# Kernel tuning notes

Measured on AMD Instinct MI355X. Metric: run time of the kernel, lower is better.

The kernel has to match this reference:

```python
import jax, jax.numpy as jnp
import numpy as np

NOPE = 128          # qk_nope_head_dim
ROPE = 64           # qk_rope_head_dim
KV_LORA = 512       # kv_lora_rank
SCALE = (KV_LORA + ROPE) ** (-0.5)


def setup_inputs() -> dict:
    key = jax.random.key(0)
    k1, k2, k3, k4, k5 = jax.random.split(key, 5)
    T, H, K, S = 512, 128, 512, 8192
    q = jax.random.normal(k1, (T, H, NOPE + ROPE), dtype=jnp.float32)
    kv_cache = jax.random.normal(k2, (S, KV_LORA + ROPE), dtype=jnp.float32)
    topk_indices = jax.random.randint(k3, (T, K), 0, S, dtype=jnp.int32)
    k_b_proj_trans = jax.random.normal(k4, (H, KV_LORA, NOPE), dtype=jnp.float32) * 0.02
    v_b_proj = jax.random.normal(k5, (H, 128, KV_LORA), dtype=jnp.float32) * 0.02
    return {"q": q, "kv_cache": kv_cache, "topk_indices": topk_indices,
            "k_b_proj_trans": k_b_proj_trans, "v_b_proj": v_b_proj}


def reference(q, kv_cache, topk_indices, k_b_proj_trans, v_b_proj):
    # q: [T, H, 192]; kv_cache: [S, 576]; topk_indices: [T, K]
    q_nope, q_rope = q[..., :NOPE], q[..., NOPE:]
    # bmm_out(q_nope_t, k_b_proj_trans.transpose(1,2)): [T,H,128] x [H,512,128] -> [T,H,512]
    q_lat = jnp.einsum('thd,hkd->thk', q_nope, k_b_proj_trans)
    q_concat = jnp.concatenate([q_lat, q_rope], axis=-1)        # [T, H, 576]
    # sparse MLA: gather selected latent KV per token
    kv_sel = kv_cache[topk_indices]                              # [T, K, 576]
    scores = jnp.einsum('thc,tkc->thk', q_concat, kv_sel) * SCALE
    p = jax.nn.softmax(scores, axis=-1)                          # [T, H, K]
    attn_lat = jnp.einsum('thk,tkc->thc', p, kv_sel[..., :KV_LORA])  # [T, H, 512]
    # bmm_out(attn_lat_t, v_b_proj.transpose(1,2)): [T,H,512] x [H,512,128] -> [T,H,128]
    out = jnp.einsum('thc,hvc->thv', attn_lat, v_b_proj)
    return out
```

## Files before the change

kernel.cpp:

```cpp
#include <hip/hip_runtime.h>
#include <stdint.h>


#define SCALE 0.041666666666666664f

typedef __bf16 bf16x8 __attribute__((ext_vector_type(8)));
typedef float floatx4 __attribute__((ext_vector_type(4)));

static __device__ __forceinline__ unsigned short f2bf(float f) {
  unsigned int u = __builtin_bit_cast(unsigned int, f);
  u += 0x7FFF + ((u >> 16) & 1);
  return (unsigned short)(u >> 16);
}
static __device__ __forceinline__ float bf2f(unsigned short h) {
  unsigned int u = ((unsigned int)h) << 16;
  return __builtin_bit_cast(float, u);
}
static __device__ __forceinline__ unsigned int pack2(float lo, float hi) {
  return (unsigned int)f2bf(lo) | ((unsigned int)f2bf(hi) << 16);
}
static __device__ __forceinline__ void ldsdma16(const void* g, void* l) {
  __builtin_amdgcn_global_load_lds(
      (const __attribute__((address_space(1))) void*)g,
      (__attribute__((address_space(3))) void*)l, 16, 0, 0);
}
static __device__ __forceinline__ void stage8_f32(const float* __restrict__ src,
                                                  unsigned short* dst) {
  const float4* s4 = reinterpret_cast<const float4*>(src);
  float4 v0 = s4[0], v1 = s4[1];
  uint4 o;
  o.x = pack2(v0.x, v0.y); o.y = pack2(v0.z, v0.w);
  o.z = pack2(v1.x, v1.y); o.w = pack2(v1.z, v1.w);
  *reinterpret_cast<uint4*>(dst) = o;
}

static __device__ __forceinline__ void mfma_4x4(const unsigned short* As,
                                                const unsigned short* Bs,
                                                int wm, int wn, int l15, int quad,
                                                floatx4 acc[4][4]) {
  bf16x8 af[4], bfr[4];
#pragma unroll
  for (int i = 0; i < 4; ++i)
    af[i] = *reinterpret_cast<const bf16x8*>(&As[(wm + i * 16 + l15) * 32 + quad * 8]);
#pragma unroll
  for (int j = 0; j < 4; ++j)
    bfr[j] = *reinterpret_cast<const bf16x8*>(&Bs[(wn + j * 16 + l15) * 32 + quad * 8]);
#pragma unroll
  for (int i = 0; i < 4; ++i)
#pragma unroll
    for (int j = 0; j < 4; ++j)
      acc[i][j] = __builtin_amdgcn_mfma_f32_16x16x32_bf16(af[i], bfr[j], acc[i][j], 0, 0, 0);
}

__global__ void prep(const float* __restrict__ kv, unsigned short* __restrict__ kvb,
                     const float* __restrict__ q, unsigned short* __restrict__ qc) {
  int b = blockIdx.x;
  if (b < 4608) {
    int i = b * 256 + threadIdx.x;
    float4 v = reinterpret_cast<const float4*>(kv)[i];
    ushort4 o;
    o.x = f2bf(v.x); o.y = f2bf(v.y); o.z = f2bf(v.z); o.w = f2bf(v.w);
    reinterpret_cast<ushort4*>(kvb)[i] = o;
  } else {
    int i = (b - 4608) * 256 + threadIdx.x;
    int r = i & 63;
    int th = i >> 6;
    qc[(size_t)th * 576 + 512 + r] = f2bf(q[(size_t)th * 192 + 128 + r] * SCALE);
  }
}

__global__ __launch_bounds__(256) void qlat_gemm(const float* __restrict__ q,
                                                 const float* __restrict__ kb,
                                                 unsigned short* __restrict__ qc) {
  const int h = blockIdx.x;
  const int tm = (blockIdx.y & 3) * 128;
  const int tn = (blockIdx.y >> 2) * 128;
  __shared__ __align__(16) unsigned short As[128 * 32];
  __shared__ __align__(16) unsigned short Bs[128 * 32];
  const int tid = threadIdx.x;
  const int lane = tid & 63, wave = tid >> 6;
  const int wm = (wave & 1) * 64, wn = (wave >> 1) * 64;
  const int l15 = lane & 15, quad = lane >> 4;
  const int r0 = tid >> 2, cg = tid & 3;
  const float* a0 = q + ((size_t)(tm + r0) * 128 + h) * 192 + cg * 8;
  const float* a1 = q + ((size_t)(tm + r0 + 64) * 128 + h) * 192 + cg * 8;
  const float* b0 = kb + ((size_t)h * 512 + tn + r0) * 128 + cg * 8;
  const float* b1 = b0 + (size_t)64 * 128;
  floatx4 acc[4][4] = {};
  for (int ks = 0; ks < 4; ++ks) {
    stage8_f32(a0 + ks * 32, &As[tid * 8]);
    stage8_f32(a1 + ks * 32, &As[2048 + tid * 8]);
    stage8_f32(b0 + ks * 32, &Bs[tid * 8]);
    stage8_f32(b1 + ks * 32, &Bs[2048 + tid * 8]);
    __syncthreads();
    mfma_4x4(As, Bs, wm, wn, l15, quad, acc);
    __syncthreads();
  }
#pragma unroll
  for (int i = 0; i < 4; ++i) {
    const int row = wm + i * 16 + quad * 4;
#pragma unroll
    for (int j = 0; j < 4; ++j) {
      const int col = wn + j * 16 + l15;
#pragma unroll
      for (int r = 0; r < 4; ++r) {
        const int t = tm + row + r;
        qc[((size_t)t * 128 + h) * 576 + tn + col] = f2bf(acc[i][j][r] * SCALE);
      }
    }
  }
}

__global__ __launch_bounds__(256) void scores_gemm(const unsigned short* __restrict__ qc,
                                                   const unsigned short* __restrict__ kvb,
                                                   const int* __restrict__ topk,
                                                   unsigned short* __restrict__ P) {
  const int t = blockIdx.x;
  const int tn = blockIdx.y * 128;
  __shared__ __align__(16) unsigned short As[128 * 32];
  __shared__ __align__(16) unsigned short Bs[128 * 32];
  const int tid = threadIdx.x;
  const int lane = tid & 63, wave = tid >> 6;
  const int wm = (wave & 1) * 64, wn = (wave >> 1) * 64;
  const int l15 = lane & 15, quad = lane >> 4;
  const int r0 = tid >> 2, cg = tid & 3;
  const unsigned short* a0 = qc + ((size_t)t * 128 + r0) * 576 + cg * 8;
  const unsigned short* a1 = a0 + (size_t)64 * 576;
  const int idx0 = topk[t * 512 + tn + r0];
  const int idx1 = topk[t * 512 + tn + r0 + 64];
  const unsigned short* b0 = kvb + (size_t)idx0 * 576 + cg * 8;
  const unsigned short* b1 = kvb + (size_t)idx1 * 576 + cg * 8;
  floatx4 acc[4][4] = {};
  for (int ks = 0; ks < 18; ++ks) {
    ldsdma16(a0 + ks * 32, &As[tid * 8]);
    ldsdma16(a1 + ks * 32, &As[2048 + tid * 8]);
    ldsdma16(b0 + ks * 32, &Bs[tid * 8]);
    ldsdma16(b1 + ks * 32, &Bs[2048 + tid * 8]);
    __syncthreads();
    mfma_4x4(As, Bs, wm, wn, l15, quad, acc);
    __syncthreads();
  }
#pragma unroll
  for (int i = 0; i < 4; ++i) {
    const int row = wm + i * 16 + quad * 4;
#pragma unroll
    for (int j = 0; j < 4; ++j) {
      const int col = tn + wn + j * 16 + l15;
#pragma unroll
      for (int r = 0; r < 4; ++r)
        P[((size_t)t * 128 + row + r) * 512 + col] = f2bf(acc[i][j][r]);
    }
  }
}

__global__ __launch_bounds__(256) void softmax_rows(const unsigned short* __restrict__ Pin,
                                                    unsigned short* __restrict__ P2) {
  const int row = blockIdx.x * 4 + (threadIdx.x >> 6);
  const int t = row >> 7, h = row & 127;
  const int lane = threadIdx.x & 63;
  const unsigned short* rp = Pin + (size_t)row * 512 + lane * 8;
  uint4 raw = *reinterpret_cast<const uint4*>(rp);
  unsigned int w[4] = {raw.x, raw.y, raw.z, raw.w};
  float f[8];
  float mx = -1e30f;
#pragma unroll
  for (int i = 0; i < 8; ++i) {
    f[i] = bf2f((unsigned short)((w[i >> 1] >> ((i & 1) * 16)) & 0xFFFF));
    mx = fmaxf(mx, f[i]);
  }
#pragma unroll
  for (int off = 32; off; off >>= 1) mx = fmaxf(mx, __shfl_xor(mx, off, 64));
  float s = 0.f;
#pragma unroll
  for (int i = 0; i < 8; ++i) { f[i] = __expf(f[i] - mx); s += f[i]; }
#pragma unroll
  for (int off = 32; off; off >>= 1) s += __shfl_xor(s, off, 64);
  const float inv = 1.0f / s;
  uint4 o;
  o.x = pack2(f[0] * inv, f[1] * inv);
  o.y = pack2(f[2] * inv, f[3] * inv);
  o.z = pack2(f[4] * inv, f[5] * inv);
  o.w = pack2(f[6] * inv, f[7] * inv);
  unsigned short* wp =
      P2 + (((size_t)t * 16 + (lane >> 2)) * 128 + h) * 32 + (lane & 3) * 8;
  *reinterpret_cast<uint4*>(wp) = o;
}

#define BSTRIDE 40
__global__ __launch_bounds__(256) void attn_gemm(const unsigned short* __restrict__ P2,
                                                 const unsigned short* __restrict__ kvb,
                                                 const int* __restrict__ topk,
                                                 unsigned short* __restrict__ alat) {
  const int t = blockIdx.x;
  const int tn = blockIdx.y * 128;
  __shared__ __align__(16) unsigned short St[2][32 * 128];
  __shared__ __align__(16) unsigned short Bs[128 * BSTRIDE];
  const int tid = threadIdx.x;
  const int lane = tid & 63, wave = tid >> 6;
  const int wm = (wave & 1) * 64, wn = (wave >> 1) * 64;
  const int l15 = lane & 15, quad = lane >> 4;
  const int key0 = tid >> 4;
  const int cs = tid & 15;
  const int kgT = tid & 3;
  const int cp = tid >> 2;
  const int* tkrow = topk + t * 512;
  const unsigned short* a_base =
      P2 + ((size_t)t * 16 * 128 + wm + l15) * 32 + quad * 8;
  floatx4 acc[4][4] = {};
  bf16x8 a_cur[4], a_nxt[4];
  {
    const int i0 = tkrow[key0];
    const int i1 = tkrow[16 + key0];
    ldsdma16(kvb + (size_t)i0 * 576 + tn + cs * 8, &St[0][tid * 8]);
    ldsdma16(kvb + (size_t)i1 * 576 + tn + cs * 8, &St[0][2048 + tid * 8]);
#pragma unroll
    for (int i = 0; i < 4; ++i)
      a_cur[i] = *reinterpret_cast<const bf16x8*>(a_base + (size_t)i * 16 * 32);
  }
  __syncthreads();
  int cur = 0;
  for (int ks = 0; ks < 16; ++ks) {
    unsigned int w[8];
#pragma unroll
    for (int i = 0; i < 8; ++i)
      w[i] = *reinterpret_cast<const unsigned int*>(
          &St[cur][(kgT * 8 + i) * 128 + cp * 2]);
    unsigned short r0[8], r1[8];
#pragma unroll
    for (int i = 0; i < 8; ++i) {
      r0[i] = (unsigned short)(w[i] & 0xFFFF);
      r1[i] = (unsigned short)(w[i] >> 16);
    }
    *reinterpret_cast<uint4*>(&Bs[(2 * cp) * BSTRIDE + kgT * 8]) =
        *reinterpret_cast<const uint4*>(r0);
    *reinterpret_cast<uint4*>(&Bs[(2 * cp + 1) * BSTRIDE + kgT * 8]) =
        *reinterpret_cast<const uint4*>(r1);
    __syncthreads();
    if (ks < 15) {
      const int i0 = tkrow[(ks + 1) * 32 + key0];
      const int i1 = tkrow[(ks + 1) * 32 + 16 + key0];
      ldsdma16(kvb + (size_t)i0 * 576 + tn + cs * 8, &St[cur ^ 1][tid * 8]);
      ldsdma16(kvb + (size_t)i1 * 576 + tn + cs * 8, &St[cur ^ 1][2048 + tid * 8]);
#pragma unroll
      for (int i = 0; i < 4; ++i)
        a_nxt[i] = *reinterpret_cast<const bf16x8*>(
            a_base + ((size_t)(ks + 1) * 128 + i * 16) * 32);
    }
    bf16x8 bfr[4];
#pragma unroll
    for (int j = 0; j < 4; ++j)
      bfr[j] = *reinterpret_cast<const bf16x8*>(
          &Bs[(wn + j * 16 + l15) * BSTRIDE + quad * 8]);
#pragma unroll
    for (int i = 0; i < 4; ++i)
#pragma unroll
      for (int j = 0; j < 4; ++j)
        acc[i][j] =
            __builtin_amdgcn_mfma_f32_16x16x32_bf16(a_cur[i], bfr[j], acc[i][j], 0, 0, 0);
    __syncthreads();
#pragma unroll
    for (int i = 0; i < 4; ++i) a_cur[i] = a_nxt[i];
    cur ^= 1;
  }
#pragma unroll
  for (int i = 0; i < 4; ++i) {
    const int row = wm + i * 16 + quad * 4;
#pragma unroll
    for (int j = 0; j < 4; ++j) {
      const int col = tn + wn + j * 16 + l15;
#pragma unroll
      for (int r = 0; r < 4; ++r)
        alat[((size_t)(row + r) * 512 + t) * 512 + col] = f2bf(acc[i][j][r]);
    }
  }
}

__global__ __launch_bounds__(256) void out_gemm(const unsigned short* __restrict__ alat,
                                                const float* __restrict__ vb,
                                                float* __restrict__ out) {
  const int h = blockIdx.x;
  const int tm = blockIdx.y * 128;
  __shared__ __align__(16) unsigned short As[128 * 32];
  __shared__ __align__(16) unsigned short Bs[128 * 32];
  const int tid = threadIdx.x;
  const int lane = tid & 63, wave = tid >> 6;
  const int wm = (wave & 1) * 64, wn = (wave >> 1) * 64;
  const int l15 = lane & 15, quad = lane >> 4;
  const int r0 = tid >> 2, cg = tid & 3;
  const unsigned short* a0 = alat + ((size_t)h * 512 + tm + r0) * 512 + cg * 8;
  const unsigned short* a1 = a0 + (size_t)64 * 512;
  const float* b0 = vb + ((size_t)h * 128 + r0) * 512 + cg * 8;
  const float* b1 = b0 + (size_t)64 * 512;
  floatx4 acc[4][4] = {};
  for (int ks = 0; ks < 16; ++ks) {
    ldsdma16(a0 + ks * 32, &As[tid * 8]);
    ldsdma16(a1 + ks * 32, &As[2048 + tid * 8]);
    stage8_f32(b0 + ks * 32, &Bs[tid * 8]);
    stage8_f32(b1 + ks * 32, &Bs[2048 + tid * 8]);
    __syncthreads();
    mfma_4x4(As, Bs, wm, wn, l15, quad, acc);
    __syncthreads();
  }
#pragma unroll
  for (int i = 0; i < 4; ++i) {
    const int row = wm + i * 16 + quad * 4;
#pragma unroll
    for (int j = 0; j < 4; ++j) {
      const int col = wn + j * 16 + l15;
#pragma unroll
      for (int r = 0; r < 4; ++r) {
        const int t = tm + row + r;
        out[((size_t)t * 128 + h) * 128 + col] = acc[i][j][r];
      }
    }
  }
}

extern "C" void kernel_launch(void* const* d_in, const int* in_sizes, int n_in,
                              void* d_out, int out_size, void* d_ws, size_t ws_size,
                              hipStream_t stream) {
  const float* q = (const float*)d_in[0];
  const float* kv = (const float*)d_in[1];
  const int* topk = (const int*)d_in[2];
  const float* kb = (const float*)d_in[3];
  const float* vb = (const float*)d_in[4];
  float* out = (float*)d_out;

  char* ws = (char*)d_ws;
  unsigned short* kvb = (unsigned short*)ws;
  unsigned short* qc = (unsigned short*)(ws + 9437184);
  unsigned short* P = (unsigned short*)(ws + 9437184 + 75497472);
  unsigned short* P2 = qc;
  unsigned short* alat = P;

  prep<<<dim3(20992), dim3(256), 0, stream>>>(kv, kvb, q, qc);
  qlat_gemm<<<dim3(128, 16), dim3(256), 0, stream>>>(q, kb, qc);
  scores_gemm<<<dim3(512, 4), dim3(256), 0, stream>>>(qc, kvb, topk, P);
  softmax_rows<<<dim3(16384), dim3(256), 0, stream>>>(P, P2);
  attn_gemm<<<dim3(512, 4), dim3(256), 0, stream>>>(P2, kvb, topk, alat);
  out_gemm<<<dim3(128, 4), dim3(256), 0, stream>>>(alat, vb, out);
}
```

Before: 395.8 us.

## Double-buffer scores GEMM and use LDS transpose reads in attention GEMM

The scores GEMM now double-buffers its A/B LDS tiles, so the async global-to-LDS copies for the next K-step overlap the MFMAs on the current one, with one barrier per iteration instead of two. The attention GEMM drops the manual LDS transpose pass and its extra Bs buffer and barrier. It instead reads B fragments directly with ds_read_b64_tr_b16 from a new layout of the gathered KV tile, and prefetches topk indices one step ahead. Risks are the inline-asm offsets and layout being wrong, the hardcoded lgkmcnt wait, and the extra LDS use in the scores kernel lowering occupancy.

```diff
diff --git a/kernel.cpp b/kernel.cpp
--- a/kernel.cpp
+++ b/kernel.cpp
@@ -6,6 +6,8 @@
 
 typedef __bf16 bf16x8 __attribute__((ext_vector_type(8)));
 typedef float floatx4 __attribute__((ext_vector_type(4)));
+typedef unsigned int uint32x2 __attribute__((ext_vector_type(2)));
+typedef unsigned int uint32x4 __attribute__((ext_vector_type(4)));
 
 static __device__ __forceinline__ unsigned short f2bf(float f) {
   unsigned int u = __builtin_bit_cast(unsigned int, f);
@@ -24,6 +26,13 @@
       (const __attribute__((address_space(1))) void*)g,
       (__attribute__((address_space(3))) void*)l, 16, 0, 0);
 }
+static __device__ __forceinline__ unsigned int lds_addr(const void* p) {
+  return (unsigned int)(unsigned long long)(
+      (__attribute__((address_space(3))) const void*)p);
+}
+#define TR64(dst, addr, OFF) \
+  asm volatile("ds_read_b64_tr_b16 %0, %1 offset:" OFF : "=v"(dst) : "v"(addr))
+
 static __device__ __forceinline__ void stage8_f32(const float* __restrict__ src,
                                                   unsigned short* dst) {
   const float4* s4 = reinterpret_cast<const float4*>(src);
@@ -117,8 +126,8 @@
                                                    unsigned short* __restrict__ P) {
   const int t = blockIdx.x;
   const int tn = blockIdx.y * 128;
-  __shared__ __align__(16) unsigned short As[128 * 32];
-  __shared__ __align__(16) unsigned short Bs[128 * 32];
+  __shared__ __align__(16) unsigned short As[2][128 * 32];
+  __shared__ __align__(16) unsigned short Bs[2][128 * 32];
   const int tid = threadIdx.x;
   const int lane = tid & 63, wave = tid >> 6;
   const int wm = (wave & 1) * 64, wn = (wave >> 1) * 64;
@@ -131,14 +140,22 @@
   const unsigned short* b0 = kvb + (size_t)idx0 * 576 + cg * 8;
   const unsigned short* b1 = kvb + (size_t)idx1 * 576 + cg * 8;
   floatx4 acc[4][4] = {};
+  ldsdma16(a0, &As[0][tid * 8]);
+  ldsdma16(a1, &As[0][2048 + tid * 8]);
+  ldsdma16(b0, &Bs[0][tid * 8]);
+  ldsdma16(b1, &Bs[0][2048 + tid * 8]);
+  __syncthreads();
+  int cur = 0;
   for (int ks = 0; ks < 18; ++ks) {
-    ldsdma16(a0 + ks * 32, &As[tid * 8]);
-    ldsdma16(a1 + ks * 32, &As[2048 + tid * 8]);
-    ldsdma16(b0 + ks * 32, &Bs[tid * 8]);
-    ldsdma16(b1 + ks * 32, &Bs[2048 + tid * 8]);
-    __syncthreads();
-    mfma_4x4(As, Bs, wm, wn, l15, quad, acc);
-    __syncthreads();
+    if (ks < 17) {
+      ldsdma16(a0 + (ks + 1) * 32, &As[cur ^ 1][tid * 8]);
+      ldsdma16(a1 + (ks + 1) * 32, &As[cur ^ 1][2048 + tid * 8]);
+      ldsdma16(b0 + (ks + 1) * 32, &Bs[cur ^ 1][tid * 8]);
+      ldsdma16(b1 + (ks + 1) * 32, &Bs[cur ^ 1][2048 + tid * 8]);
+    }
+    mfma_4x4(As[cur], Bs[cur], wm, wn, l15, quad, acc);
+    __syncthreads();
+    cur ^= 1;
   }
 #pragma unroll
   for (int i = 0; i < 4; ++i) {
@@ -186,7 +203,6 @@
   *reinterpret_cast<uint4*>(wp) = o;
 }
 
-#define BSTRIDE 40
 __global__ __launch_bounds__(256) void attn_gemm(const unsigned short* __restrict__ P2,
                                                  const unsigned short* __restrict__ kvb,
                                                  const int* __restrict__ topk,
@@ -194,25 +210,26 @@
   const int t = blockIdx.x;
   const int tn = blockIdx.y * 128;
   __shared__ __align__(16) unsigned short St[2][32 * 128];
-  __shared__ __align__(16) unsigned short Bs[128 * BSTRIDE];
   const int tid = threadIdx.x;
   const int lane = tid & 63, wave = tid >> 6;
   const int wm = (wave & 1) * 64, wn = (wave >> 1) * 64;
   const int l15 = lane & 15, quad = lane >> 4;
-  const int key0 = tid >> 4;
-  const int cs = tid & 15;
-  const int kgT = tid & 3;
-  const int cp = tid >> 2;
+  const int keyA = wave * 4 + ((tid >> 1) & 3);
+  const int cA = ((tid >> 3) & 7) * 16 + (tid & 1) * 8;
   const int* tkrow = topk + t * 512;
   const unsigned short* a_base =
       P2 + ((size_t)t * 16 * 128 + wm + l15) * 32 + quad * 8;
+  const unsigned int tra0 = lds_addr(&St[0][0]) + quad * 2048 + wn * 8 + l15 * 8;
   floatx4 acc[4][4] = {};
   bf16x8 a_cur[4], a_nxt[4];
+  int i0p, i1p;
   {
-    const int i0 = tkrow[key0];
-    const int i1 = tkrow[16 + key0];
-    ldsdma16(kvb + (size_t)i0 * 576 + tn + cs * 8, &St[0][tid * 8]);
-    ldsdma16(kvb + (size_t)i1 * 576 + tn + cs * 8, &St[0][2048 + tid * 8]);
+    const int i0 = tkrow[keyA];
+    const int i1 = tkrow[16 + keyA];
+    ldsdma16(kvb + (size_t)i0 * 576 + tn + cA, &St[0][tid * 8]);
+    ldsdma16(kvb + (size_t)i1 * 576 + tn + cA, &St[0][2048 + tid * 8]);
+    i0p = tkrow[32 + keyA];
+    i1p = tkrow[48 + keyA];
 #pragma unroll
     for (int i = 0; i < 4; ++i)
       a_cur[i] = *reinterpret_cast<const bf16x8*>(a_base + (size_t)i * 16 * 32);
@@ -220,37 +237,38 @@
   __syncthreads();
   int cur = 0;
   for (int ks = 0; ks < 16; ++ks) {
-    unsigned int w[8];
-#pragma unroll
-    for (int i = 0; i < 8; ++i)
-      w[i] = *reinterpret_cast<const unsigned int*>(
-          &St[cur][(kgT * 8 + i) * 128 + cp * 2]);
-    unsigned short r0[8], r1[8];
-#pragma unroll
-    for (int i = 0; i < 8; ++i) {
-      r0[i] = (unsigned short)(w[i] & 0xFFFF);
-      r1[i] = (unsigned short)(w[i] >> 16);
-    }
-    *reinterpret_cast<uint4*>(&Bs[(2 * cp) * BSTRIDE + kgT * 8]) =
-        *reinterpret_cast<const uint4*>(r0);
-    *reinterpret_cast<uint4*>(&Bs[(2 * cp + 1) * BSTRIDE + kgT * 8]) =
-        *reinterpret_cast<const uint4*>(r1);
-    __syncthreads();
+    const unsigned int tra = tra0 + cur * 8192;
+    uint32x2 r00, r01, r10, r11, r20, r21, r30, r31;
+    TR64(r00, tra, "0");   TR64(r01, tra, "1024");
+    TR64(r10, tra, "128"); TR64(r11, tra, "1152");
+    TR64(r20, tra, "256"); TR64(r21, tra, "1280");
+    TR64(r30, tra, "384"); TR64(r31, tra, "1408");
     if (ks < 15) {
-      const int i0 = tkrow[(ks + 1) * 32 + key0];
-      const int i1 = tkrow[(ks + 1) * 32 + 16 + key0];
-      ldsdma16(kvb + (size_t)i0 * 576 + tn + cs * 8, &St[cur ^ 1][tid * 8]);
-      ldsdma16(kvb + (size_t)i1 * 576 + tn + cs * 8, &St[cur ^ 1][2048 + tid * 8]);
+      ldsdma16(kvb + (size_t)i0p * 576 + tn + cA, &St[cur ^ 1][tid * 8]);
+      ldsdma16(kvb + (size_t)i1p * 576 + tn + cA, &St[cur ^ 1][2048 + tid * 8]);
 #pragma unroll
       for (int i = 0; i < 4; ++i)
         a_nxt[i] = *reinterpret_cast<const bf16x8*>(
             a_base + ((size_t)(ks + 1) * 128 + i * 16) * 32);
-    }
+      if (ks < 14) {
+        i0p = tkrow[(ks + 2) * 32 + keyA];
+        i1p = tkrow[(ks + 2) * 32 + 16 + keyA];
+      }
+    }
+    asm volatile("s_waitcnt lgkmcnt(0)");
+    __builtin_amdgcn_sched_barrier(0);
     bf16x8 bfr[4];
-#pragma unroll
-    for (int j = 0; j < 4; ++j)
-      bfr[j] = *reinterpret_cast<const bf16x8*>(
-          &Bs[(wn + j * 16 + l15) * BSTRIDE + quad * 8]);
+    {
+      uint32x4 w;
+      w.x = r00.x; w.y = r00.y; w.z = r01.x; w.w = r01.y;
+      bfr[0] = __builtin_bit_cast(bf16x8, w);
+      w.x = r10.x; w.y = r10.y; w.z = r11.x; w.w = r11.y;
+      bfr[1] = __builtin_bit_cast(bf16x8, w);
+      w.x = r20.x; w.y = r20.y; w.z = r21.x; w.w = r21.y;
+      bfr[2] = __builtin_bit_cast(bf16x8, w);
+      w.x = r30.x; w.y = r30.y; w.z = r31.x; w.w = r31.y;
+      bfr[3] = __builtin_bit_cast(bf16x8, w);
+    }
 #pragma unroll
     for (int i = 0; i < 4; ++i)
 #pragma unroll
```

After: 385.4 us. 1.03x faster.
